# Optimization experiments

Measured on AMD Instinct MI355X. Metric: run time of the kernel, lower is better.

## Reference

```python
import jax, jax.numpy as jnp
import numpy as np

KEEP_RATIO = 0.7

def setup_inputs() -> dict:
    key = jax.random.key(0)
    k1, k2, k3 = jax.random.split(key, 3)
    B, N, D = 4, 16384, 1024
    H = D // 4
    x = jax.random.normal(k1, (B, N, D), dtype=jnp.float32)
    W1 = jax.random.normal(k2, (D, H), dtype=jnp.float32) * (1.0 / np.sqrt(D))
    b1 = jnp.zeros((H,), dtype=jnp.float32)
    W2 = jax.random.normal(k3, (H, 1), dtype=jnp.float32) * (1.0 / np.sqrt(H))
    b2 = jnp.zeros((1,), dtype=jnp.float32)
    return {"x": x, "W1": W1, "b1": b1, "W2": W2, "b2": b2}

def reference(x, W1, b1, W2, b2):
    # x: [B, N, D]
    B, N, D = x.shape
    k = int(N * KEEP_RATIO)  # static under jit
    h = jax.nn.relu(jnp.einsum('bnd,dh->bnh', x, W1) + b1)
    scores = jax.nn.sigmoid(jnp.einsum('bnh,ho->bno', h, W2) + b2)  # [B, N, 1]
    score_values = scores[..., 0]  # [B, N]
    x_weighted = x * scores  # [B, N, D]
    _, top_k_indices = jax.lax.top_k(score_values, k)  # [B, k]
    top_k_indices = jnp.sort(top_k_indices, axis=1)
    x_kept = jnp.take_along_axis(x_weighted, top_k_indices[:, :, None], axis=1)  # [B, k, D]
    sparsity_loss = -jnp.mean(jnp.abs(score_values - 0.5))
    return x_kept, sparsity_loss
```

## Files before the change

### kernel.cpp

```cpp
#include <hip/hip_runtime.h>
#include <hip/hip_bf16.h>
#include <math.h>

#define N_TOK 16384
#define BATCH 4
#define DIM   1024
#define HID   256
#define KEEP  11468
#define MROWS 65536
#define BK    64
#define NKT   (DIM / BK)
#define DELTA 6e-3f
#define WCAP  4096

typedef __attribute__((ext_vector_type(8))) short bf16x8;
typedef __attribute__((ext_vector_type(4))) float f32x4;

__device__ inline unsigned bf16_rne(float f) {
    unsigned u = __float_as_uint(f);
    return (u + 0x7FFFu + ((u >> 16) & 1u)) >> 16;
}

#define GLDS16(gp, lp) __builtin_amdgcn_global_load_lds( \
    (const __attribute__((address_space(1))) void*)(gp), \
    (__attribute__((address_space(3))) void*)(lp), 16, 0, 0)

__global__ __launch_bounds__(256) void prep_kernel(
    const float* __restrict__ W1, ushort* __restrict__ Wpk)
{
    const int kt = blockIdx.x;
    for (int idx = threadIdx.x; idx < 2048; idx += 256) {
        const int lane = idx & 63;
        const int g    = idx >> 6;
        const int h    = (g & 15) * 16 + (lane & 15);
        const int kb   = kt * 64 + (g >> 4) * 32 + (lane >> 4) * 8;
        ushort v[8];
#pragma unroll
        for (int j = 0; j < 8; ++j)
            v[j] = (ushort)bf16_rne(W1[(size_t)(kb + j) * HID + h]);
        *(uint4*)(Wpk + ((size_t)(kt * 32 + g) * 64 + lane) * 8) = *(uint4*)v;
    }
}

__global__ __launch_bounds__(512, 2) void score_mfma(
    const float* __restrict__ x, const ushort* __restrict__ Wpk,
    const float* __restrict__ b1, const float* __restrict__ W2,
    const float* __restrict__ b2, float* __restrict__ scores,
    float* __restrict__ partials)
{
    __shared__ ushort As[2][128 * 64];
    __shared__ ushort Bs[2][32 * 512];
    __shared__ float zbuf[128][4];
    __shared__ float red[128];

    const int t    = threadIdx.x;
    const int lane = t & 63;
    const int w    = t >> 6;
    const int wr   = w >> 2;
    const int wc   = w & 3;
    const int l15  = lane & 15;
    const int lk   = lane >> 4;
    const size_t row0 = (size_t)blockIdx.x * 128;

    const int arow = t >> 2;
    const int aq   = t & 3;
    const float* xbase = x + (row0 + arow) * DIM + aq * 16;

    f32x4 acc[4][4];
#pragma unroll
    for (int rf = 0; rf < 4; ++rf)
#pragma unroll
        for (int cf = 0; cf < 4; ++cf) acc[rf][cf] = (f32x4){0.f, 0.f, 0.f, 0.f};

    float pf[16];
#define LOADA(KT) { const float* xp = xbase + (KT) * BK; \
        *(float4*)&pf[0]  = ((const float4*)xp)[0]; \
        *(float4*)&pf[4]  = ((const float4*)xp)[1]; \
        *(float4*)&pf[8]  = ((const float4*)xp)[2]; \
        *(float4*)&pf[12] = ((const float4*)xp)[3]; }
#define STOREA(BUF) { \
        ushort hb[16]; \
        _Pragma("unroll") \
        for (int j = 0; j < 16; ++j) hb[j] = (ushort)bf16_rne(pf[j]); \
        char* base_ = (char*)&As[BUF][0] + arow * 128; \
        const int swz_ = (arow & 7) << 4; \
        *(uint4*)(base_ + ((aq * 32) ^ swz_))      = *(uint4*)&hb[0]; \
        *(uint4*)(base_ + ((aq * 32 + 16) ^ swz_)) = *(uint4*)&hb[8]; }
#define LOADB(KT, BUF) { \
        _Pragma("unroll") \
        for (int i = 0; i < 4; ++i) { \
            const int g_ = w * 4 + i; \
            GLDS16(Wpk + (((size_t)(KT) * 32 + g_) * 64 + lane) * 8, \
                   &Bs[BUF][g_ * 512 + lane * 8]); \
        } }

    LOADB(0, 0);
    LOADA(0);
    STOREA(0);
    __syncthreads();

    for (int kt = 0; kt < NKT; ++kt) {
        const int cur = kt & 1;
        const int nxt = cur ^ 1;
        if (kt < NKT - 1) {
            LOADB(kt + 1, nxt);
            LOADA(kt + 1);
        }
#pragma unroll
        for (int ks = 0; ks < 2; ++ks) {
            bf16x8 Af[4];
#pragma unroll
            for (int rf = 0; rf < 4; ++rf) {
                const int row = wr * 64 + rf * 16 + l15;
                const int kb  = (ks * 64 + lk * 16) ^ ((row & 7) << 4);
                Af[rf] = *(const bf16x8*)((const char*)&As[cur][0] + row * 128 + kb);
            }
#pragma unroll
            for (int cf = 0; cf < 4; ++cf) {
                const int g = ks * 16 + wc * 4 + cf;
                const bf16x8 Bf = *(const bf16x8*)&Bs[cur][g * 512 + lane * 8];
                acc[0][cf] = __builtin_amdgcn_mfma_f32_16x16x32_bf16(Af[0], Bf, acc[0][cf], 0, 0, 0);
                acc[1][cf] = __builtin_amdgcn_mfma_f32_16x16x32_bf16(Af[1], Bf, acc[1][cf], 0, 0, 0);
                acc[2][cf] = __builtin_amdgcn_mfma_f32_16x16x32_bf16(Af[2], Bf, acc[2][cf], 0, 0, 0);
                acc[3][cf] = __builtin_amdgcn_mfma_f32_16x16x32_bf16(Af[3], Bf, acc[3][cf], 0, 0, 0);
            }
        }
        if (kt < NKT - 1) STOREA(nxt);
        __syncthreads();
    }

    float b1r[4], w2r[4];
#pragma unroll
    for (int cf = 0; cf < 4; ++cf) {
        const int col = wc * 64 + cf * 16 + l15;
        b1r[cf] = b1[col];
        w2r[cf] = W2[col];
    }
#pragma unroll
    for (int rf = 0; rf < 4; ++rf) {
#pragma unroll
        for (int j = 0; j < 4; ++j) {
            float z = 0.f;
#pragma unroll
            for (int cf = 0; cf < 4; ++cf)
                z = fmaf(fmaxf(acc[rf][cf][j] + b1r[cf], 0.f), w2r[cf], z);
            z += __shfl_xor(z, 1);
            z += __shfl_xor(z, 2);
            z += __shfl_xor(z, 4);
            z += __shfl_xor(z, 8);
            if (l15 == 0) zbuf[wr * 64 + rf * 16 + lk * 4 + j][wc] = z;
        }
    }
    __syncthreads();
    if (t < 128) {
        const float z = (zbuf[t][0] + zbuf[t][1]) + (zbuf[t][2] + zbuf[t][3]) + b2[0];
        const float s = 1.f / (1.f + expf(-z));
        scores[row0 + t] = s;
        red[t] = fabsf(s - 0.5f);
    }
    __syncthreads();
    for (int off = 64; off > 0; off >>= 1) {
        if (t < off) red[t] += red[t + off];
        __syncthreads();
    }
    if (t == 0) partials[blockIdx.x] = red[0];
}

__global__ __launch_bounds__(1024) void fixfind_kernel(
    const float* __restrict__ scores, int* __restrict__ winList,
    int* __restrict__ winCnt)
{
    const int b    = blockIdx.x;
    const int t    = threadIdx.x;
    const int lane = t & 63;
    const int wid  = t >> 6;
    __shared__ unsigned red[17];
    __shared__ unsigned wsum[16];

    float sv[16];
    unsigned bits[16];
    const float4* sp = (const float4*)(scores + (size_t)b * N_TOK + t * 16);
#pragma unroll
    for (int j = 0; j < 4; ++j) {
        const float4 v = sp[j];
        sv[j * 4 + 0] = v.x; sv[j * 4 + 1] = v.y;
        sv[j * 4 + 2] = v.z; sv[j * 4 + 3] = v.w;
    }
#pragma unroll
    for (int j = 0; j < 16; ++j) bits[j] = __float_as_uint(sv[j]);

    auto countGE = [&](unsigned v) -> unsigned {
        unsigned c = 0;
#pragma unroll
        for (int j = 0; j < 16; ++j) c += (bits[j] >= v) ? 1u : 0u;
        c += __shfl_xor(c, 32); c += __shfl_xor(c, 16); c += __shfl_xor(c, 8);
        c += __shfl_xor(c, 4);  c += __shfl_xor(c, 2);  c += __shfl_xor(c, 1);
        if (lane == 0) red[wid] = c;
        __syncthreads();
        if (t == 0) {
            unsigned s = 0;
            for (int w = 0; w < 16; ++w) s += red[w];
            red[16] = s;
        }
        __syncthreads();
        return red[16];
    };

    unsigned lo = 0u, hi = 0x40000000u;
    while (hi - lo > 1u) {
        const unsigned mid = (lo + hi) >> 1;
        if (countGE(mid) >= KEEP) lo = mid; else hi = mid;
    }
    const float sT = __uint_as_float(lo);

    int cnt = 0;
    bool inw[16];
#pragma unroll
    for (int j = 0; j < 16; ++j) {
        inw[j] = fabsf(sv[j] - sT) <= DELTA;
        cnt += inw[j] ? 1 : 0;
    }
    unsigned inc = (unsigned)cnt;
#pragma unroll
    for (int off = 1; off < 64; off <<= 1) {
        const unsigned n = __shfl_up(inc, off);
        if (lane >= off) inc += n;
    }
    const unsigned excl = inc - (unsigned)cnt;
    if (lane == 63) wsum[wid] = inc;
    __syncthreads();
    if (t == 0) {
        unsigned s = 0;
        for (int w = 0; w < 16; ++w) { const unsigned tmp = wsum[w]; wsum[w] = s; s += tmp; }
        winCnt[b] = (int)(s > WCAP ? WCAP : s);
    }
    __syncthreads();
    unsigned pos = wsum[wid] + excl;
#pragma unroll
    for (int j = 0; j < 16; ++j) {
        if (inw[j]) {
            if (pos < WCAP) winList[b * WCAP + pos] = t * 16 + j;
            ++pos;
        }
    }
}

__global__ __launch_bounds__(1024) void fix2_kernel(
    const float* __restrict__ x, const float* __restrict__ W1,
    const float* __restrict__ b1, const float* __restrict__ W2,
    const float* __restrict__ b2, float* __restrict__ scores,
    const int* __restrict__ winList, const int* __restrict__ winCnt)
{
    __shared__ float xrT[1024][8];
    __shared__ float part[4][8][256];
    __shared__ int rows[8];

    const int t = threadIdx.x;
    int c[4], cum[5];
    cum[0] = 0;
    for (int b = 0; b < 4; ++b) {
        int cc = winCnt[b];
        if (cc > WCAP) cc = WCAP;
        if (cc < 0) cc = 0;
        c[b] = cc;
        cum[b + 1] = cum[b] + ((cc + 7) >> 3);
    }
    for (int g = blockIdx.x; g < cum[4]; g += gridDim.x) {
        int b = 0;
        while (g >= cum[b + 1]) ++b;
        const int gi   = g - cum[b];
        const int nval = min(8, c[b] - gi * 8);
        if (t < 8)
            rows[t] = winList[b * WCAP + gi * 8 + (t < nval ? t : 0)];
        __syncthreads();
        {
            const int r = t >> 7, c0 = (t & 127) * 8;
            const float* xp = x + ((size_t)b * N_TOK + rows[r]) * DIM + c0;
            const float4 a = ((const float4*)xp)[0], bq = ((const float4*)xp)[1];
            xrT[c0 + 0][r] = a.x;  xrT[c0 + 1][r] = a.y;
            xrT[c0 + 2][r] = a.z;  xrT[c0 + 3][r] = a.w;
            xrT[c0 + 4][r] = bq.x; xrT[c0 + 5][r] = bq.y;
            xrT[c0 + 6][r] = bq.z; xrT[c0 + 7][r] = bq.w;
        }
        __syncthreads();
        const int h = t & 255, q = t >> 8;
        float a8[8];
#pragma unroll
        for (int r = 0; r < 8; ++r) a8[r] = 0.f;
        const int k0 = q * 256;
        for (int k = 0; k < 256; ++k) {
            const float wv = W1[(size_t)(k0 + k) * HID + h];
            const float4 xa = *(const float4*)&xrT[k0 + k][0];
            const float4 xb = *(const float4*)&xrT[k0 + k][4];
            a8[0] = fmaf(xa.x, wv, a8[0]); a8[1] = fmaf(xa.y, wv, a8[1]);
            a8[2] = fmaf(xa.z, wv, a8[2]); a8[3] = fmaf(xa.w, wv, a8[3]);
            a8[4] = fmaf(xb.x, wv, a8[4]); a8[5] = fmaf(xb.y, wv, a8[5]);
            a8[6] = fmaf(xb.z, wv, a8[6]); a8[7] = fmaf(xb.w, wv, a8[7]);
        }
#pragma unroll
        for (int r = 0; r < 8; ++r) part[q][r][h] = a8[r];
        __syncthreads();
        const int wid = t >> 6, lane = t & 63;
        if (wid < 8) {
            const int r = wid;
            float v = 0.f;
#pragma unroll
            for (int i = 0; i < 4; ++i) {
                const int hc = i * 64 + lane;
                float hv = (part[0][r][hc] + part[1][r][hc]) + (part[2][r][hc] + part[3][r][hc]);
                hv = fmaxf(hv + b1[hc], 0.f);
                v = fmaf(hv, W2[hc], v);
            }
            v += __shfl_xor(v, 32); v += __shfl_xor(v, 16); v += __shfl_xor(v, 8);
            v += __shfl_xor(v, 4);  v += __shfl_xor(v, 2);  v += __shfl_xor(v, 1);
            if (lane == 0 && r < nval)
                scores[(size_t)b * N_TOK + rows[r]] = 1.f / (1.f + expf(-(v + b2[0])));
        }
        __syncthreads();
    }
}

__global__ __launch_bounds__(1024) void select_kernel(
    const float* __restrict__ scores, int* __restrict__ idxList)
{
    const int b    = blockIdx.x;
    const int t    = threadIdx.x;
    const int lane = t & 63;
    const int wid  = t >> 6;
    __shared__ unsigned red[17];

    unsigned bits[16];
    const float4* sp = (const float4*)(scores + (size_t)b * N_TOK + t * 16);
#pragma unroll
    for (int j = 0; j < 4; ++j) {
        const float4 v = sp[j];
        bits[j * 4 + 0] = __float_as_uint(v.x);
        bits[j * 4 + 1] = __float_as_uint(v.y);
        bits[j * 4 + 2] = __float_as_uint(v.z);
        bits[j * 4 + 3] = __float_as_uint(v.w);
    }

    auto countGE = [&](unsigned v) -> unsigned {
        unsigned c = 0;
#pragma unroll
        for (int j = 0; j < 16; ++j) c += (bits[j] >= v) ? 1u : 0u;
        c += __shfl_xor(c, 32); c += __shfl_xor(c, 16); c += __shfl_xor(c, 8);
        c += __shfl_xor(c, 4);  c += __shfl_xor(c, 2);  c += __shfl_xor(c, 1);
        if (lane == 0) red[wid] = c;
        __syncthreads();
        if (t == 0) {
            unsigned s = 0;
            for (int w = 0; w < 16; ++w) s += red[w];
            red[16] = s;
        }
        __syncthreads();
        return red[16];
    };

    unsigned lo = 0u, hi = 0x40000000u;
    while (hi - lo > 1u) {
        const unsigned mid = (lo + hi) >> 1;
        if (countGE(mid) >= KEEP) lo = mid; else hi = mid;
    }
    const unsigned T    = lo;
    const unsigned cGT  = countGE(T + 1u);
    const unsigned need = KEEP - cGT;

    unsigned pre[16];
    unsigned run = 0;
#pragma unroll
    for (int j = 0; j < 16; ++j) {
        pre[j] = run;
        const unsigned gt = (bits[j] > T) ? 1u : 0u;
        const unsigned eq = (bits[j] == T) ? 1u : 0u;
        run += gt | (eq << 16);
    }
    unsigned inc = run;
#pragma unroll
    for (int off = 1; off < 64; off <<= 1) {
        const unsigned n = __shfl_up(inc, off);
        if (lane >= off) inc += n;
    }
    const unsigned waveExcl = inc - run;
    if (lane == 63) red[wid] = inc;
    __syncthreads();
    if (t == 0) {
        unsigned s = 0;
        for (int w = 0; w < 16; ++w) { const unsigned tmp = red[w]; red[w] = s; s += tmp; }
    }
    __syncthreads();
    const unsigned base = red[wid] + waveExcl;

#pragma unroll
    for (int j = 0; j < 16; ++j) {
        const unsigned pe    = base + pre[j];
        const unsigned tieR  = pe >> 16;
        const unsigned posGT = pe & 0xFFFFu;
        const bool gt = bits[j] > T;
        const bool eq = bits[j] == T;
        if (gt || (eq && tieR < need)) {
            const unsigned pos = posGT + (tieR < need ? tieR : need);
            idxList[(size_t)b * KEEP + pos] = t * 16 + j;
        }
    }
}

__global__ __launch_bounds__(256) void gather_kernel(
    const float* __restrict__ x, const float* __restrict__ scores,
    const int* __restrict__ idxList, float* __restrict__ out)
{
    const int t = threadIdx.x;
#pragma unroll
    for (int q = 0; q < 4; ++q) {
        const int orow = blockIdx.x * 4 + q;
        const int b    = orow / KEEP;
        const int idx  = idxList[orow];
        const float s  = scores[(size_t)b * N_TOK + idx];
        const float4 v = *(const float4*)(x + (((size_t)b * N_TOK + idx) << 10) + t * 4);
        float4 o;
        o.x = v.x * s; o.y = v.y * s; o.z = v.z * s; o.w = v.w * s;
        *(float4*)(out + ((size_t)orow << 10) + t * 4) = o;
    }
}

__global__ __launch_bounds__(256) void loss_kernel(
    const float* __restrict__ partials, float* __restrict__ outLoss)
{
    __shared__ float red[256];
    const int t = threadIdx.x;
    red[t] = partials[t] + partials[t + 256];
    __syncthreads();
    for (int off = 128; off > 0; off >>= 1) {
        if (t < off) red[t] += red[t + off];
        __syncthreads();
    }
    if (t == 0) outLoss[0] = -(red[0] / (float)MROWS);
}

extern "C" void kernel_launch(void* const* d_in, const int* in_sizes, int n_in,
                              void* d_out, int out_size, void* d_ws, size_t ws_size,
                              hipStream_t stream)
{
    const float* x  = (const float*)d_in[0];
    const float* W1 = (const float*)d_in[1];
    const float* b1 = (const float*)d_in[2];
    const float* W2 = (const float*)d_in[3];
    const float* b2 = (const float*)d_in[4];
    float* out = (float*)d_out;

    char* ws = (char*)d_ws;
    float* scores   = (float*)ws;
    float* partials = (float*)(ws + 262144);
    int*   idxList  = (int*)(ws + 266240);
    ushort* Wpk     = (ushort*)(ws + 458752);
    int*   winList  = (int*)(ws + 983040);
    int*   winCnt   = (int*)(ws + 1048576);

    prep_kernel<<<NKT, 256, 0, stream>>>(W1, Wpk);
    score_mfma<<<MROWS / 128, 512, 0, stream>>>(x, Wpk, b1, W2, b2, scores, partials);
    loss_kernel<<<1, 256, 0, stream>>>(partials, out + (size_t)BATCH * KEEP * DIM);
    fixfind_kernel<<<BATCH, 1024, 0, stream>>>(scores, winList, winCnt);
    fix2_kernel<<<256, 1024, 0, stream>>>(x, W1, b1, W2, b2, scores, winList, winCnt);
    select_kernel<<<BATCH, 1024, 0, stream>>>(scores, idxList);
    gather_kernel<<<KEEP, 256, 0, stream>>>(x, scores, idxList, out);
}
```

Baseline: 240.1 us.

## Double M-tile of scoring GEMM to 256 rows per block and restructure MFMA loop

Raises the score GEMM tile from 128 to 256 rows per block, so each wave holds an 8x4 accumulator grid. Each loaded W1 fragment is now reused across twice as many rows, which halves the B-tile global/LDS traffic per output. A-tile conversion now packs bf16 pairs into 32-bit words, and a sched_barrier is placed after the prefetch. It also replaces the serial 16-way final sum in the countGE binary searches with a wave shuffle reduction, and the loss kernel now reads 256 partials. In exchange, LDS and register use per block roughly double, which may lower occupancy below the two blocks per CU the launch bounds request, and the grid shrinks to 256 blocks.

```diff
diff --git a/kernel.cpp b/kernel.cpp
--- a/kernel.cpp
+++ b/kernel.cpp
@@ -8,8 +8,8 @@
 #define HID   256
 #define KEEP  11468
 #define MROWS 65536
-#define BK    64
-#define NKT   (DIM / BK)
+#define BM    256
+#define NK2   16
 #define DELTA 6e-3f
 #define WCAP  4096
 
@@ -48,10 +48,10 @@
     const float* __restrict__ b2, float* __restrict__ scores,
     float* __restrict__ partials)
 {
-    __shared__ ushort As[2][128 * 64];
+    __shared__ ushort As[2][BM * 64];
     __shared__ ushort Bs[2][32 * 512];
-    __shared__ float zbuf[128][4];
-    __shared__ float red[128];
+    __shared__ float zbuf[BM][4];
+    __shared__ float red[BM];
 
     const int t    = threadIdx.x;
     const int lane = t & 63;
@@ -60,38 +60,40 @@
     const int wc   = w & 3;
     const int l15  = lane & 15;
     const int lk   = lane >> 4;
-    const size_t row0 = (size_t)blockIdx.x * 128;
-
-    const int arow = t >> 2;
-    const int aq   = t & 3;
-    const float* xbase = x + (row0 + arow) * DIM + aq * 16;
-
-    f32x4 acc[4][4];
-#pragma unroll
-    for (int rf = 0; rf < 4; ++rf)
+    const size_t row0 = (size_t)blockIdx.x * BM;
+
+    const int arow  = t >> 1;
+    const int ahalf = t & 1;
+    const float* xbase = x + (row0 + arow) * DIM + ahalf * 32;
+    const int aswz = (arow & 7) << 4;
+    const ushort* bb = Wpk;
+
+    f32x4 acc[8][4];
+#pragma unroll
+    for (int rf = 0; rf < 8; ++rf)
 #pragma unroll
         for (int cf = 0; cf < 4; ++cf) acc[rf][cf] = (f32x4){0.f, 0.f, 0.f, 0.f};
 
-    float pf[16];
-#define LOADA(KT) { const float* xp = xbase + (KT) * BK; \
-        *(float4*)&pf[0]  = ((const float4*)xp)[0]; \
-        *(float4*)&pf[4]  = ((const float4*)xp)[1]; \
-        *(float4*)&pf[8]  = ((const float4*)xp)[2]; \
-        *(float4*)&pf[12] = ((const float4*)xp)[3]; }
+    float pf[32];
+
+#define LOADA(KT) { const float4* xp = (const float4*)(xbase + (size_t)(KT) * 64); \
+        _Pragma("unroll") \
+        for (int j = 0; j < 8; ++j) *(float4*)&pf[j * 4] = xp[j]; }
 #define STOREA(BUF) { \
-        ushort hb[16]; \
+        unsigned hb[16]; \
         _Pragma("unroll") \
-        for (int j = 0; j < 16; ++j) hb[j] = (ushort)bf16_rne(pf[j]); \
+        for (int j = 0; j < 16; ++j) \
+            hb[j] = bf16_rne(pf[2 * j]) | (bf16_rne(pf[2 * j + 1]) << 16); \
         char* base_ = (char*)&As[BUF][0] + arow * 128; \
-        const int swz_ = (arow & 7) << 4; \
-        *(uint4*)(base_ + ((aq * 32) ^ swz_))      = *(uint4*)&hb[0]; \
-        *(uint4*)(base_ + ((aq * 32 + 16) ^ swz_)) = *(uint4*)&hb[8]; }
+        _Pragma("unroll") \
+        for (int j = 0; j < 4; ++j) \
+            *(uint4*)(base_ + ((ahalf * 64 + j * 16) ^ aswz)) = *(uint4*)&hb[j * 4]; }
 #define LOADB(KT, BUF) { \
         _Pragma("unroll") \
         for (int i = 0; i < 4; ++i) { \
-            const int g_ = w * 4 + i; \
-            GLDS16(Wpk + (((size_t)(KT) * 32 + g_) * 64 + lane) * 8, \
-                   &Bs[BUF][g_ * 512 + lane * 8]); \
+            const int line_ = w * 4 + i; \
+            GLDS16(Wpk + (((size_t)(KT) * 32 + line_) * 64 + lane) * 8, \
+                   &Bs[BUF][line_ * 512 + lane * 8]); \
         } }
 
     LOADB(0, 0);
@@ -99,33 +101,35 @@
     STOREA(0);
     __syncthreads();
 
-    for (int kt = 0; kt < NKT; ++kt) {
+    for (int kt = 0; kt < NK2; ++kt) {
         const int cur = kt & 1;
         const int nxt = cur ^ 1;
-        if (kt < NKT - 1) {
+        if (kt < NK2 - 1) {
+            LOADA(kt + 1);
             LOADB(kt + 1, nxt);
-            LOADA(kt + 1);
-        }
+        }
+        __builtin_amdgcn_sched_barrier(0);
 #pragma unroll
         for (int ks = 0; ks < 2; ++ks) {
-            bf16x8 Af[4];
-#pragma unroll
-            for (int rf = 0; rf < 4; ++rf) {
-                const int row = wr * 64 + rf * 16 + l15;
-                const int kb  = (ks * 64 + lk * 16) ^ ((row & 7) << 4);
-                Af[rf] = *(const bf16x8*)((const char*)&As[cur][0] + row * 128 + kb);
+            bf16x8 Af[8];
+#pragma unroll
+            for (int rf = 0; rf < 8; ++rf) {
+                const int r = wr * 128 + rf * 16 + l15;
+                const int kb = (ks * 64 + lk * 16) ^ ((r & 7) << 4);
+                Af[rf] = *(const bf16x8*)((const char*)&As[cur][0] + r * 128 + kb);
             }
-#pragma unroll
-            for (int cf = 0; cf < 4; ++cf) {
-                const int g = ks * 16 + wc * 4 + cf;
-                const bf16x8 Bf = *(const bf16x8*)&Bs[cur][g * 512 + lane * 8];
-                acc[0][cf] = __builtin_amdgcn_mfma_f32_16x16x32_bf16(Af[0], Bf, acc[0][cf], 0, 0, 0);
-                acc[1][cf] = __builtin_amdgcn_mfma_f32_16x16x32_bf16(Af[1], Bf, acc[1][cf], 0, 0, 0);
-                acc[2][cf] = __builtin_amdgcn_mfma_f32_16x16x32_bf16(Af[2], Bf, acc[2][cf], 0, 0, 0);
-                acc[3][cf] = __builtin_amdgcn_mfma_f32_16x16x32_bf16(Af[3], Bf, acc[3][cf], 0, 0, 0);
-            }
-        }
-        if (kt < NKT - 1) STOREA(nxt);
+            bf16x8 Bf[4];
+#pragma unroll
+            for (int cf = 0; cf < 4; ++cf)
+                Bf[cf] = *(const bf16x8*)&Bs[cur][(ks * 16 + wc * 4 + cf) * 512 + lane * 8];
+#pragma unroll
+            for (int cf = 0; cf < 4; ++cf)
+#pragma unroll
+                for (int rf = 0; rf < 8; ++rf)
+                    acc[rf][cf] = __builtin_amdgcn_mfma_f32_16x16x32_bf16(
+                        Af[rf], Bf[cf], acc[rf][cf], 0, 0, 0);
+        }
+        if (kt < NK2 - 1) STOREA(nxt);
         __syncthreads();
     }
 
@@ -137,7 +141,7 @@
         w2r[cf] = W2[col];
     }
 #pragma unroll
-    for (int rf = 0; rf < 4; ++rf) {
+    for (int rf = 0; rf < 8; ++rf) {
 #pragma unroll
         for (int j = 0; j < 4; ++j) {
             float z = 0.f;
@@ -148,19 +152,19 @@
             z += __shfl_xor(z, 2);
             z += __shfl_xor(z, 4);
             z += __shfl_xor(z, 8);
-            if (l15 == 0) zbuf[wr * 64 + rf * 16 + lk * 4 + j][wc] = z;
-        }
-    }
-    __syncthreads();
-    if (t < 128) {
+            if (l15 == 0) zbuf[wr * 128 + rf * 16 + lk * 4 + j][wc] = z;
+        }
+    }
+    __syncthreads();
+    if (t < BM) {
         const float z = (zbuf[t][0] + zbuf[t][1]) + (zbuf[t][2] + zbuf[t][3]) + b2[0];
         const float s = 1.f / (1.f + expf(-z));
         scores[row0 + t] = s;
         red[t] = fabsf(s - 0.5f);
     }
     __syncthreads();
-    for (int off = 64; off > 0; off >>= 1) {
-        if (t < off) red[t] += red[t + off];
+    for (int off = 128; off > 0; off >>= 1) {
+        if (t < off && t + off < BM) red[t] += red[t + off];
         __syncthreads();
     }
     if (t == 0) partials[blockIdx.x] = red[0];
@@ -197,10 +201,11 @@
         c += __shfl_xor(c, 4);  c += __shfl_xor(c, 2);  c += __shfl_xor(c, 1);
         if (lane == 0) red[wid] = c;
         __syncthreads();
-        if (t == 0) {
-            unsigned s = 0;
-            for (int w = 0; w < 16; ++w) s += red[w];
-            red[16] = s;
+        if (wid == 0) {
+            unsigned s = (lane < 16) ? red[lane] : 0u;
+            s += __shfl_xor(s, 8); s += __shfl_xor(s, 4);
+            s += __shfl_xor(s, 2); s += __shfl_xor(s, 1);
+            if (lane == 0) red[16] = s;
         }
         __syncthreads();
         return red[16];
@@ -348,10 +353,11 @@
         c += __shfl_xor(c, 4);  c += __shfl_xor(c, 2);  c += __shfl_xor(c, 1);
         if (lane == 0) red[wid] = c;
         __syncthreads();
-        if (t == 0) {
-            unsigned s = 0;
-            for (int w = 0; w < 16; ++w) s += red[w];
-            red[16] = s;
+        if (wid == 0) {
+            unsigned s = (lane < 16) ? red[lane] : 0u;
+            s += __shfl_xor(s, 8); s += __shfl_xor(s, 4);
+            s += __shfl_xor(s, 2); s += __shfl_xor(s, 1);
+            if (lane == 0) red[16] = s;
         }
         __syncthreads();
         return red[16];
@@ -428,7 +434,7 @@
 {
     __shared__ float red[256];
     const int t = threadIdx.x;
-    red[t] = partials[t] + partials[t + 256];
+    red[t] = partials[t];
     __syncthreads();
     for (int off = 128; off > 0; off >>= 1) {
         if (t < off) red[t] += red[t + off];
@@ -456,8 +462,8 @@
     int*   winList  = (int*)(ws + 983040);
     int*   winCnt   = (int*)(ws + 1048576);
 
-    prep_kernel<<<NKT, 256, 0, stream>>>(W1, Wpk);
-    score_mfma<<<MROWS / 128, 512, 0, stream>>>(x, Wpk, b1, W2, b2, scores, partials);
+    prep_kernel<<<16, 256, 0, stream>>>(W1, Wpk);
+    score_mfma<<<MROWS / BM, 512, 0, stream>>>(x, Wpk, b1, W2, b2, scores, partials);
     loss_kernel<<<1, 256, 0, stream>>>(partials, out + (size_t)BATCH * KEEP * DIM);
     fixfind_kernel<<<BATCH, 1024, 0, stream>>>(scores, winList, winCnt);
     fix2_kernel<<<256, 1024, 0, stream>>>(x, W1, b1, W2, b2, scores, winList, winCnt);
```

New measurement: 239.3 us. Within noise of the previous version (-0.3%).
